# Performance work log

Measured on AMD Instinct MI355X. Metric: run time of the kernel, lower is better.

The kernel has to match this reference:

```python
import jax, jax.numpy as jnp
import numpy as np

B, C, H, W = 2, 512, 256, 256
EPS = 1e-5


def setup_inputs() -> dict:
    key = jax.random.key(0)
    ks = jax.random.split(key, 11)
    inp = {
        "x": jax.random.normal(ks[0], (B, C, H, W), dtype=jnp.float32),
        "w1": jax.random.normal(ks[1], (C, 1, H, 1), dtype=jnp.float32) * 0.05,
        "w2": jax.random.normal(ks[2], (C, 1, 1, W), dtype=jnp.float32) * 0.05,
        "g1": jax.random.uniform(ks[3], (C,), dtype=jnp.float32) + 0.5,
        "b1": jax.random.normal(ks[4], (C,), dtype=jnp.float32) * 0.1,
        "g2": jax.random.uniform(ks[5], (C,), dtype=jnp.float32) + 0.5,
        "b2": jax.random.normal(ks[6], (C,), dtype=jnp.float32) * 0.1,
        "lw1": jax.random.normal(ks[7], (2 * C, C), dtype=jnp.float32) * 0.02,
        "lb1": jax.random.normal(ks[8], (2 * C,), dtype=jnp.float32) * 0.02,
        "lw2": jax.random.normal(ks[9], (C, 2 * C), dtype=jnp.float32) * 0.02,
        "lb2": jax.random.normal(ks[10], (C,), dtype=jnp.float32) * 0.02,
    }
    return inp


def _dwconv(x, k):
    # depthwise conv, VALID padding, stride 1; k: [C,1,kh,kw]
    return jax.lax.conv_general_dilated(
        x, k, window_strides=(1, 1), padding="VALID",
        dimension_numbers=("NCHW", "OIHW", "NCHW"),
        feature_group_count=x.shape[1])


def _bn_relu(y, gamma, beta):
    # BatchNorm2d in training mode: biased batch stats over (N,H,W)
    m = jnp.mean(y, axis=(0, 2, 3), keepdims=True)
    v = jnp.var(y, axis=(0, 2, 3), keepdims=True)
    yn = (y - m) * jax.lax.rsqrt(v + EPS)
    return jax.nn.relu(yn * gamma.reshape(1, -1, 1, 1) + beta.reshape(1, -1, 1, 1))


def reference(x, w1, w2, g1, b1, g2, b2, lw1, lb1, lw2, lb2):
    b, c, h, w = x.shape
    xl1 = _bn_relu(_dwconv(x, w1), g1, b1)  # [b,c,1,w]
    xl2 = _bn_relu(_dwconv(x, w2), g2, b2)  # [b,c,h,1]
    # per-(channel,batch) dot product; torch code stacks as [c,b,1] then views (b,c)
    dot_cb = jnp.einsum("bck,bck->cb", xl1[:, :, 0, :], xl2[:, :, :, 0])  # [c,b]
    num = dot_cb.reshape(b, c)  # faithful layout-scrambling view
    num = num @ lw1.T + lb1
    num = num @ lw2.T + lb2
    num = jax.nn.softmax(num, axis=1)  # [b,c]
    return x * num[:, :, None, None]
```

## Files before the change

### kernel.cpp

```cpp
#include <hip/hip_runtime.h>
#include <hip/hip_bf16.h>

#define Bn 2
#define Cn 512
#define Hn 256
#define Wn 256
#define EPSc 1e-5f

__global__ __launch_bounds__(256) void k1_reduce(const float* __restrict__ x,
                                                 const float* __restrict__ w1,
                                                 const float* __restrict__ w2,
                                                 float* __restrict__ s1,
                                                 float* __restrict__ s2) {
    const int bc   = blockIdx.x;
    const int c    = bc & (Cn - 1);
    const int tid  = threadIdx.x;
    const int wave = tid >> 6;
    const int lane = tid & 63;
    const float* __restrict__ xs = x + (size_t)bc * (Hn * Wn);

    __shared__ float w1s[Hn];
    __shared__ float s1buf[4][Wn];

    w1s[tid] = w1[c * Hn + tid];
    __syncthreads();

    const float4 w2v = *(const float4*)(w2 + c * Wn + lane * 4);

    float4 acc = make_float4(0.f, 0.f, 0.f, 0.f);
    #pragma unroll 2
    for (int h = wave; h < Hn; h += 4) {
        float4 v = *(const float4*)(xs + h * Wn + lane * 4);
        float wh = w1s[h];
        acc.x += v.x * wh; acc.y += v.y * wh;
        acc.z += v.z * wh; acc.w += v.w * wh;
        float p = v.x * w2v.x + v.y * w2v.y + v.z * w2v.z + v.w * w2v.w;
        #pragma unroll
        for (int off = 32; off; off >>= 1) p += __shfl_xor(p, off, 64);
        if (lane == 0) s2[bc * Hn + h] = p;
    }
    ((float4*)(&s1buf[wave][0]))[lane] = acc;
    __syncthreads();
    s1[bc * Wn + tid] = s1buf[0][tid] + s1buf[1][tid] + s1buf[2][tid] + s1buf[3][tid];
}

__global__ __launch_bounds__(256) void k2_bn_dot(const float* __restrict__ s1,
                                                 const float* __restrict__ s2,
                                                 const float* __restrict__ g1,
                                                 const float* __restrict__ b1,
                                                 const float* __restrict__ g2,
                                                 const float* __restrict__ b2,
                                                 float* __restrict__ numv) {
    const int c = blockIdx.x * 4 + (threadIdx.x >> 6);
    const int lane = threadIdx.x & 63;
    if (c >= Cn) return;

    float v1[2][4], v2[2][4];
    float sum1 = 0.f, sq1 = 0.f, sum2 = 0.f, sq2 = 0.f;
    #pragma unroll
    for (int b = 0; b < 2; b++) {
        #pragma unroll
        for (int m = 0; m < 4; m++) {
            float a = s1[(b * Cn + c) * Wn + lane + 64 * m];
            float d = s2[(b * Cn + c) * Hn + lane + 64 * m];
            v1[b][m] = a; v2[b][m] = d;
            sum1 += a; sq1 += a * a;
            sum2 += d; sq2 += d * d;
        }
    }
    #pragma unroll
    for (int off = 32; off; off >>= 1) {
        sum1 += __shfl_xor(sum1, off, 64);
        sq1  += __shfl_xor(sq1,  off, 64);
        sum2 += __shfl_xor(sum2, off, 64);
        sq2  += __shfl_xor(sq2,  off, 64);
    }
    const float inv = 1.0f / 512.0f;
    float m1 = sum1 * inv, m2 = sum2 * inv;
    float r1 = rsqrtf(sq1 * inv - m1 * m1 + EPSc);
    float r2 = rsqrtf(sq2 * inv - m2 * m2 + EPSc);
    float G1 = g1[c], B1 = b1[c], G2 = g2[c], B2 = b2[c];

    #pragma unroll
    for (int b = 0; b < 2; b++) {
        float d = 0.f;
        #pragma unroll
        for (int m = 0; m < 4; m++) {
            float a = fmaxf((v1[b][m] - m1) * r1 * G1 + B1, 0.f);
            float e = fmaxf((v2[b][m] - m2) * r2 * G2 + B2, 0.f);
            d += a * e;
        }
        #pragma unroll
        for (int off = 32; off; off >>= 1) d += __shfl_xor(d, off, 64);
        if (lane == 0) numv[c * 2 + b] = d;
    }
}

__global__ __launch_bounds__(256) void k3_fc1(const float* __restrict__ numv,
                                              const float* __restrict__ lw1,
                                              const float* __restrict__ lb1,
                                              float* __restrict__ h1) {
    const int wid  = blockIdx.x * 4 + (threadIdx.x >> 6);
    const int lane = threadIdx.x & 63;
    const int bb = wid >> 10, j = wid & 1023;
    const float* __restrict__ row = lw1 + (size_t)j * Cn;
    const float* __restrict__ nv  = numv + bb * Cn;
    float p = 0.f;
    #pragma unroll
    for (int m = 0; m < 2; m++) {
        float4 a = *(const float4*)(row + lane * 4 + m * 256);
        float4 n = *(const float4*)(nv  + lane * 4 + m * 256);
        p += a.x * n.x + a.y * n.y + a.z * n.z + a.w * n.w;
    }
    #pragma unroll
    for (int off = 32; off; off >>= 1) p += __shfl_xor(p, off, 64);
    if (lane == 0) h1[bb * 1024 + j] = p + lb1[j];
}

__global__ __launch_bounds__(256) void k4_fc2(const float* __restrict__ h1,
                                              const float* __restrict__ lw2,
                                              const float* __restrict__ lb2,
                                              float* __restrict__ h2) {
    const int wid  = blockIdx.x * 4 + (threadIdx.x >> 6);
    const int lane = threadIdx.x & 63;
    const int bb = wid >> 9, c = wid & 511;
    const float* __restrict__ row = lw2 + (size_t)c * 1024;
    const float* __restrict__ hv  = h1 + bb * 1024;
    float p = 0.f;
    #pragma unroll
    for (int m = 0; m < 4; m++) {
        float4 a = *(const float4*)(row + lane * 4 + m * 256);
        float4 n = *(const float4*)(hv  + lane * 4 + m * 256);
        p += a.x * n.x + a.y * n.y + a.z * n.z + a.w * n.w;
    }
    #pragma unroll
    for (int off = 32; off; off >>= 1) p += __shfl_xor(p, off, 64);
    if (lane == 0) h2[bb * Cn + c] = p + lb2[c];
}

__global__ __launch_bounds__(512) void k5_softmax(const float* __restrict__ h2,
                                                  float* __restrict__ scale) {
    __shared__ float red[512];
    const int bb = blockIdx.x, t = threadIdx.x;
    float v = h2[bb * Cn + t];
    red[t] = v;
    __syncthreads();
    for (int s = 256; s; s >>= 1) {
        if (t < s) red[t] = fmaxf(red[t], red[t + s]);
        __syncthreads();
    }
    float mx = red[0];
    __syncthreads();
    float e = expf(v - mx);
    red[t] = e;
    __syncthreads();
    for (int s = 256; s; s >>= 1) {
        if (t < s) red[t] += red[t + s];
        __syncthreads();
    }
    scale[bb * Cn + t] = e / red[0];
}

__global__ __launch_bounds__(256) void k6_scale(const float* __restrict__ x,
                                                const float* __restrict__ scale,
                                                float* __restrict__ out, int n4) {
    int i = blockIdx.x * 256 + threadIdx.x;
    const int stride = gridDim.x * 256;
    for (; i < n4; i += stride) {
        float4 v = ((const float4*)x)[i];
        float s = scale[i >> 14];
        ((float4*)out)[i] = make_float4(v.x * s, v.y * s, v.z * s, v.w * s);
    }
}

extern "C" void kernel_launch(void* const* d_in, const int* in_sizes, int n_in,
                              void* d_out, int out_size, void* d_ws, size_t ws_size,
                              hipStream_t stream) {
    const float* x   = (const float*)d_in[0];
    const float* w1  = (const float*)d_in[1];
    const float* w2  = (const float*)d_in[2];
    const float* g1  = (const float*)d_in[3];
    const float* b1  = (const float*)d_in[4];
    const float* g2  = (const float*)d_in[5];
    const float* b2  = (const float*)d_in[6];
    const float* lw1 = (const float*)d_in[7];
    const float* lb1 = (const float*)d_in[8];
    const float* lw2 = (const float*)d_in[9];
    const float* lb2 = (const float*)d_in[10];
    float* out = (float*)d_out;

    float* ws   = (float*)d_ws;
    float* s1   = ws;
    float* s2   = ws + 262144;
    float* numv = ws + 524288;
    float* h1   = ws + 525312;
    float* h2   = ws + 527360;
    float* scl  = ws + 528384;

    k1_reduce<<<Bn * Cn, 256, 0, stream>>>(x, w1, w2, s1, s2);
    k2_bn_dot<<<Cn / 4, 256, 0, stream>>>(s1, s2, g1, b1, g2, b2, numv);
    k3_fc1<<<512, 256, 0, stream>>>(numv, lw1, lb1, h1);
    k4_fc2<<<256, 256, 0, stream>>>(h1, lw2, lb2, h2);
    k5_softmax<<<Bn, 512, 0, stream>>>(h2, scl);

    const int n4 = (Bn * Cn * Hn * Wn) / 4;
    k6_scale<<<4096, 256, 0, stream>>>(x, scl, out, n4);
}
```

Measured before the change: 526.3 us.

## Fuse reduction with BN-dot per channel and softmax into scale kernel

The first reduction now runs one 512-thread block per channel that covers both batches. It computes the BatchNorm statistics, ReLU and dot product in shared memory, so the s1/s2 workspace round trip and the separate BN kernel go away. Softmax is recomputed redundantly by every block of the scaling kernel, which removes one launch. The output stores are now nontemporal. In exchange there are half as many blocks in the streaming reduction, which could lower occupancy, and each of the 4096 scaling blocks does a small redundant softmax.

```diff
diff --git a/kernel.cpp b/kernel.cpp
--- a/kernel.cpp
+++ b/kernel.cpp
@@ -7,29 +7,39 @@
 #define Wn 256
 #define EPSc 1e-5f
 
-__global__ __launch_bounds__(256) void k1_reduce(const float* __restrict__ x,
-                                                 const float* __restrict__ w1,
-                                                 const float* __restrict__ w2,
-                                                 float* __restrict__ s1,
-                                                 float* __restrict__ s2) {
-    const int bc   = blockIdx.x;
-    const int c    = bc & (Cn - 1);
+typedef float f32x4 __attribute__((ext_vector_type(4)));
+
+__global__ __launch_bounds__(512) void k1_fused(const float* __restrict__ x,
+                                                const float* __restrict__ w1,
+                                                const float* __restrict__ w2,
+                                                const float* __restrict__ g1v,
+                                                const float* __restrict__ b1v,
+                                                const float* __restrict__ g2v,
+                                                const float* __restrict__ b2v,
+                                                float* __restrict__ numv) {
+    const int c    = blockIdx.x;
     const int tid  = threadIdx.x;
-    const int wave = tid >> 6;
+    const int wv   = tid >> 6;
     const int lane = tid & 63;
-    const float* __restrict__ xs = x + (size_t)bc * (Hn * Wn);
+    const int bb   = wv >> 2;
+    const int wq   = wv & 3;
 
     __shared__ float w1s[Hn];
-    __shared__ float s1buf[4][Wn];
-
-    w1s[tid] = w1[c * Hn + tid];
+    __shared__ float s1buf[8][Wn];
+    __shared__ float s2s[2][Hn];
+    __shared__ float redbuf[8][4];
+    __shared__ float stats[4];
+    __shared__ float dred[8];
+
+    if (tid < Hn) w1s[tid] = w1[c * Hn + tid];
     __syncthreads();
 
     const float4 w2v = *(const float4*)(w2 + c * Wn + lane * 4);
+    const float* __restrict__ xs = x + (size_t)(bb * Cn + c) * (Hn * Wn);
 
     float4 acc = make_float4(0.f, 0.f, 0.f, 0.f);
     #pragma unroll 2
-    for (int h = wave; h < Hn; h += 4) {
+    for (int h = wq; h < Hn; h += 4) {
         float4 v = *(const float4*)(xs + h * Wn + lane * 4);
         float wh = w1s[h];
         acc.x += v.x * wh; acc.y += v.y * wh;
@@ -37,37 +47,17 @@
         float p = v.x * w2v.x + v.y * w2v.y + v.z * w2v.z + v.w * w2v.w;
         #pragma unroll
         for (int off = 32; off; off >>= 1) p += __shfl_xor(p, off, 64);
-        if (lane == 0) s2[bc * Hn + h] = p;
-    }
-    ((float4*)(&s1buf[wave][0]))[lane] = acc;
-    __syncthreads();
-    s1[bc * Wn + tid] = s1buf[0][tid] + s1buf[1][tid] + s1buf[2][tid] + s1buf[3][tid];
-}
-
-__global__ __launch_bounds__(256) void k2_bn_dot(const float* __restrict__ s1,
-                                                 const float* __restrict__ s2,
-                                                 const float* __restrict__ g1,
-                                                 const float* __restrict__ b1,
-                                                 const float* __restrict__ g2,
-                                                 const float* __restrict__ b2,
-                                                 float* __restrict__ numv) {
-    const int c = blockIdx.x * 4 + (threadIdx.x >> 6);
-    const int lane = threadIdx.x & 63;
-    if (c >= Cn) return;
-
-    float v1[2][4], v2[2][4];
-    float sum1 = 0.f, sq1 = 0.f, sum2 = 0.f, sq2 = 0.f;
-    #pragma unroll
-    for (int b = 0; b < 2; b++) {
-        #pragma unroll
-        for (int m = 0; m < 4; m++) {
-            float a = s1[(b * Cn + c) * Wn + lane + 64 * m];
-            float d = s2[(b * Cn + c) * Hn + lane + 64 * m];
-            v1[b][m] = a; v2[b][m] = d;
-            sum1 += a; sq1 += a * a;
-            sum2 += d; sq2 += d * d;
-        }
-    }
+        if (lane == 0) s2s[bb][h] = p;
+    }
+    ((float4*)(&s1buf[wv][0]))[lane] = acc;
+    __syncthreads();
+
+    const int bI = tid >> 8, k = tid & 255;
+    float s1v = s1buf[bI * 4 + 0][k] + s1buf[bI * 4 + 1][k] +
+                s1buf[bI * 4 + 2][k] + s1buf[bI * 4 + 3][k];
+    float s2v = s2s[bI][k];
+
+    float sum1 = s1v, sq1 = s1v * s1v, sum2 = s2v, sq2 = s2v * s2v;
     #pragma unroll
     for (int off = 32; off; off >>= 1) {
         sum1 += __shfl_xor(sum1, off, 64);
@@ -75,25 +65,40 @@
         sum2 += __shfl_xor(sum2, off, 64);
         sq2  += __shfl_xor(sq2,  off, 64);
     }
-    const float inv = 1.0f / 512.0f;
-    float m1 = sum1 * inv, m2 = sum2 * inv;
-    float r1 = rsqrtf(sq1 * inv - m1 * m1 + EPSc);
-    float r2 = rsqrtf(sq2 * inv - m2 * m2 + EPSc);
-    float G1 = g1[c], B1 = b1[c], G2 = g2[c], B2 = b2[c];
-
-    #pragma unroll
-    for (int b = 0; b < 2; b++) {
-        float d = 0.f;
-        #pragma unroll
-        for (int m = 0; m < 4; m++) {
-            float a = fmaxf((v1[b][m] - m1) * r1 * G1 + B1, 0.f);
-            float e = fmaxf((v2[b][m] - m2) * r2 * G2 + B2, 0.f);
-            d += a * e;
+    if (lane == 0) {
+        redbuf[wv][0] = sum1; redbuf[wv][1] = sq1;
+        redbuf[wv][2] = sum2; redbuf[wv][3] = sq2;
+    }
+    __syncthreads();
+    if (tid == 0) {
+        float t1 = 0.f, t2 = 0.f, t3 = 0.f, t4 = 0.f;
+        #pragma unroll
+        for (int q = 0; q < 8; q++) {
+            t1 += redbuf[q][0]; t2 += redbuf[q][1];
+            t3 += redbuf[q][2]; t4 += redbuf[q][3];
         }
-        #pragma unroll
-        for (int off = 32; off; off >>= 1) d += __shfl_xor(d, off, 64);
-        if (lane == 0) numv[c * 2 + b] = d;
-    }
+        const float inv = 1.0f / 512.0f;
+        float m1 = t1 * inv, m2 = t3 * inv;
+        stats[0] = m1;
+        stats[1] = rsqrtf(t2 * inv - m1 * m1 + EPSc);
+        stats[2] = m2;
+        stats[3] = rsqrtf(t4 * inv - m2 * m2 + EPSc);
+    }
+    __syncthreads();
+
+    const float m1 = stats[0], r1 = stats[1], m2 = stats[2], r2 = stats[3];
+    const float G1 = g1v[c], B1 = b1v[c], G2 = g2v[c], B2 = b2v[c];
+
+    float a = fmaxf((s1v - m1) * r1 * G1 + B1, 0.f);
+    float e = fmaxf((s2v - m2) * r2 * G2 + B2, 0.f);
+    float p = a * e;
+    #pragma unroll
+    for (int off = 32; off; off >>= 1) p += __shfl_xor(p, off, 64);
+    if (lane == 0) dred[wv] = p;
+    __syncthreads();
+    if (tid < 2)
+        numv[c * 2 + tid] = dred[tid * 4 + 0] + dred[tid * 4 + 1] +
+                            dred[tid * 4 + 2] + dred[tid * 4 + 3];
 }
 
 __global__ __launch_bounds__(256) void k3_fc1(const float* __restrict__ numv,
@@ -138,38 +143,48 @@
     if (lane == 0) h2[bb * Cn + c] = p + lb2[c];
 }
 
-__global__ __launch_bounds__(512) void k5_softmax(const float* __restrict__ h2,
-                                                  float* __restrict__ scale) {
-    __shared__ float red[512];
-    const int bb = blockIdx.x, t = threadIdx.x;
-    float v = h2[bb * Cn + t];
-    red[t] = v;
-    __syncthreads();
-    for (int s = 256; s; s >>= 1) {
-        if (t < s) red[t] = fmaxf(red[t], red[t + s]);
-        __syncthreads();
-    }
-    float mx = red[0];
-    __syncthreads();
-    float e = expf(v - mx);
-    red[t] = e;
-    __syncthreads();
-    for (int s = 256; s; s >>= 1) {
-        if (t < s) red[t] += red[t + s];
-        __syncthreads();
-    }
-    scale[bb * Cn + t] = e / red[0];
-}
-
-__global__ __launch_bounds__(256) void k6_scale(const float* __restrict__ x,
-                                                const float* __restrict__ scale,
-                                                float* __restrict__ out, int n4) {
-    int i = blockIdx.x * 256 + threadIdx.x;
+__global__ __launch_bounds__(256) void k6_softmax_scale(const float* __restrict__ x,
+                                                        const float* __restrict__ h2,
+                                                        float* __restrict__ out, int n4) {
+    __shared__ float h2s[1024];
+    __shared__ float scls[1024];
+    __shared__ float mxs[2], sms[2];
+    const int t = threadIdx.x;
+
+    #pragma unroll
+    for (int j = 0; j < 4; j++) h2s[t + 256 * j] = h2[t + 256 * j];
+    __syncthreads();
+
+    const int wv = t >> 6, lane = t & 63;
+    if (wv < 2) {
+        float mx = -3.402823466e+38f;
+        #pragma unroll
+        for (int j = 0; j < 8; j++) mx = fmaxf(mx, h2s[wv * 512 + lane + 64 * j]);
+        #pragma unroll
+        for (int off = 32; off; off >>= 1) mx = fmaxf(mx, __shfl_xor(mx, off, 64));
+        float sm = 0.f;
+        #pragma unroll
+        for (int j = 0; j < 8; j++) sm += expf(h2s[wv * 512 + lane + 64 * j] - mx);
+        #pragma unroll
+        for (int off = 32; off; off >>= 1) sm += __shfl_xor(sm, off, 64);
+        if (lane == 0) { mxs[wv] = mx; sms[wv] = sm; }
+    }
+    __syncthreads();
+    #pragma unroll
+    for (int j = 0; j < 4; j++) {
+        int idx = t + 256 * j;
+        int r = idx >> 9;
+        scls[idx] = expf(h2s[idx] - mxs[r]) / sms[r];
+    }
+    __syncthreads();
+
+    int i = blockIdx.x * 256 + t;
     const int stride = gridDim.x * 256;
     for (; i < n4; i += stride) {
-        float4 v = ((const float4*)x)[i];
-        float s = scale[i >> 14];
-        ((float4*)out)[i] = make_float4(v.x * s, v.y * s, v.z * s, v.w * s);
+        f32x4 v = ((const f32x4*)x)[i];
+        float s = scls[i >> 14];
+        f32x4 r = v * s;
+        __builtin_nontemporal_store(r, ((f32x4*)out) + i);
     }
 }
 
@@ -190,19 +205,14 @@
     float* out = (float*)d_out;
 
     float* ws   = (float*)d_ws;
-    float* s1   = ws;
-    float* s2   = ws + 262144;
-    float* numv = ws + 524288;
-    float* h1   = ws + 525312;
-    float* h2   = ws + 527360;
-    float* scl  = ws + 528384;
-
-    k1_reduce<<<Bn * Cn, 256, 0, stream>>>(x, w1, w2, s1, s2);
-    k2_bn_dot<<<Cn / 4, 256, 0, stream>>>(s1, s2, g1, b1, g2, b2, numv);
+    float* numv = ws;
+    float* h1   = ws + 1024;
+    float* h2   = ws + 3072;
+
+    k1_fused<<<Cn, 512, 0, stream>>>(x, w1, w2, g1, b1, g2, b2, numv);
     k3_fc1<<<512, 256, 0, stream>>>(numv, lw1, lb1, h1);
     k4_fc2<<<256, 256, 0, stream>>>(h1, lw2, lb2, h2);
-    k5_softmax<<<Bn, 512, 0, stream>>>(h2, scl);
 
     const int n4 = (Bn * Cn * Hn * Wn) / 4;
-    k6_scale<<<4096, 256, 0, stream>>>(x, scl, out, n4);
-}
+    k6_softmax_scale<<<4096, 256, 0, stream>>>(x, h2, out, n4);
+}
```

New measurement: 508.9 us, median of 2. 3.3% less time.
